# Kernel tuning notes

Measured on AMD Instinct MI355X. Metric: run time of the kernel, lower is better.

The kernel has to match this reference:

```python
import jax, jax.numpy as jnp
import numpy as np

B, S, D = 8, 1024, 768
H = 12
DH = D // H  # 64
SCALE = 1.0 / (D ** 0.5)  # module scales by full embedding_dim, not head_dim


def setup_inputs() -> dict:
    key = jax.random.key(0)
    ks = jax.random.split(key, 7)
    std = 1.0 / np.sqrt(D)
    return {
        "x": jax.random.normal(ks[0], (B, S, D), dtype=jnp.float32),
        "Wq": jax.random.uniform(ks[1], (D, D), jnp.float32, -std, std),
        "bq": jax.random.uniform(ks[2], (D,), jnp.float32, -std, std),
        "Wk": jax.random.uniform(ks[3], (D, D), jnp.float32, -std, std),
        "bk": jax.random.uniform(ks[4], (D,), jnp.float32, -std, std),
        "Wv": jax.random.uniform(ks[5], (D, D), jnp.float32, -std, std),
        "bv": jax.random.uniform(ks[6], (D,), jnp.float32, -std, std),
    }


def reference(x, Wq, bq, Wk, bk, Wv, bv):
    b, s, d = x.shape
    # projections; torch.chunk(dim=-1) == reshape last dim to [H, DH]
    q = (x @ Wq + bq).reshape(b, s, H, DH)
    k = (x @ Wk + bk).reshape(b, s, H, DH)
    v = (x @ Wv + bv).reshape(b, s, H, DH)
    # per-head scores [b, h, s, s], scaled by sqrt(embedding_dim) per source
    scores = jnp.einsum("bqhd,bkhd->bhqk", q, k) * SCALE
    attn = jax.nn.softmax(scores, axis=-1)
    out = jnp.einsum("bhqk,bkhd->bqhd", attn, v)
    # concat heads back along last dim (order matches chunk order)
    return out.reshape(b, s, d)
```

## Files before the change

kernel.cpp:

```cpp
#include <hip/hip_runtime.h>
#include <cstdint>
#include <cstddef>

typedef unsigned short u16;
typedef unsigned int u32;
typedef unsigned char u8;

using bfx8 = __attribute__((ext_vector_type(8))) __bf16;
using floatx16 = __attribute__((ext_vector_type(16))) float;

static constexpr int kS = 1024;
static constexpr int kD = 768;
static constexpr int kH = 12;
static constexpr int kDH = 64;
#define SCALE 0.036084391824351614f

__device__ __forceinline__ u16 f2bf(float f) {
    u32 u = __float_as_uint(f);
    return (u16)((u + 0x7fffu + ((u >> 16) & 1u)) >> 16);
}

__device__ __forceinline__ void gld16(const void* g, void* l) {
    __builtin_amdgcn_global_load_lds(
        (__attribute__((address_space(1))) const u32*)g,
        (__attribute__((address_space(3))) u32*)l, 16, 0, 0);
}

__global__ __launch_bounds__(256) void cvt_x(const float* __restrict__ x, u16* __restrict__ xb) {
    int i = (blockIdx.x * 256 + threadIdx.x) * 4;
    float4 v = *(const float4*)(x + i);
    u32 lo = (u32)f2bf(v.x) | ((u32)f2bf(v.y) << 16);
    u32 hi = (u32)f2bf(v.z) | ((u32)f2bf(v.w) << 16);
    *(uint2*)(xb + i) = make_uint2(lo, hi);
}

__global__ __launch_bounds__(256) void cvt_w(const float* __restrict__ w0, const float* __restrict__ w1,
                                             const float* __restrict__ w2, u16* __restrict__ wt) {
    __shared__ float t[32][33];
    const float* W = blockIdx.z == 0 ? w0 : (blockIdx.z == 1 ? w1 : w2);
    u16* dst = wt + (size_t)blockIdx.z * kD * kD;
    int k0 = blockIdx.x * 32, n0 = blockIdx.y * 32;
    int tx = threadIdx.x, ty = threadIdx.y;
#pragma unroll
    for (int j = 0; j < 4; j++)
        t[ty + j * 8][tx] = W[(size_t)(k0 + ty + j * 8) * kD + n0 + tx];
    __syncthreads();
#pragma unroll
    for (int j = 0; j < 4; j++)
        dst[(size_t)(n0 + ty + j * 8) * kD + k0 + tx] = f2bf(t[tx][ty + j * 8]);
}

__global__ __launch_bounds__(256) void proj(const u16* __restrict__ xb, const u16* __restrict__ wt,
                                            const float* __restrict__ bq, const float* __restrict__ bk,
                                            const float* __restrict__ bvp,
                                            u16* __restrict__ qb, u16* __restrict__ kb, u16* __restrict__ vt) {
    __shared__ u16 As[128 * 64];
    __shared__ u16 Bs[128 * 64];
    int m0 = blockIdx.x * 128;
    int n0g = blockIdx.y * 128;
    int t = threadIdx.x;
    int w = t >> 6, lane = t & 63;
    int l31 = lane & 31, hi = lane >> 5;
    int wm = (w & 1) * 64, wn = (w >> 1) * 64;
    int rloc8 = lane >> 3, p8 = lane & 7;
    int chw = p8 ^ rloc8;
    const u16* Brow = wt + (size_t)n0g * kD;
    int swz = l31 & 7;
    floatx16 acc[2][2] = {};
    for (int ks = 0; ks < kD; ks += 64) {
        __syncthreads();
#pragma unroll
        for (int i = 0; i < 4; i++) {
            int j = w * 4 + i;
            int r = 8 * j + rloc8;
            gld16(xb + (size_t)(m0 + r) * kD + ks + chw * 8, &As[j * 512]);
            gld16(Brow + (size_t)r * kD + ks + chw * 8, &Bs[j * 512]);
        }
        __syncthreads();
#pragma unroll
        for (int s = 0; s < 4; s++) {
            int tc = ((s * 2 + hi) ^ swz) * 8;
            bfx8 a[2], bf[2];
#pragma unroll
            for (int i = 0; i < 2; i++) {
                a[i] = *(const bfx8*)&As[(wm + i * 32 + l31) * 64 + tc];
                bf[i] = *(const bfx8*)&Bs[(wn + i * 32 + l31) * 64 + tc];
            }
#pragma unroll
            for (int i = 0; i < 2; i++)
#pragma unroll
                for (int j = 0; j < 2; j++)
                    acc[i][j] = __builtin_amdgcn_mfma_f32_32x32x16_bf16(a[i], bf[j], acc[i][j], 0, 0, 0);
        }
    }
    int zz = blockIdx.y / 6;
    int nl0 = (blockIdx.y - zz * 6) * 128;
    const float* bias = zz == 0 ? bq : (zz == 1 ? bk : bvp);
    float mul = zz == 0 ? SCALE : 1.0f;
#pragma unroll
    for (int j = 0; j < 2; j++) {
        int nl = nl0 + wn + j * 32 + l31;
        float bb = bias[nl];
#pragma unroll
        for (int i = 0; i < 2; i++) {
            int mbase = m0 + wm + i * 32 + 4 * hi;
            if (zz < 2) {
                u16* dst = zz == 0 ? qb : kb;
#pragma unroll
                for (int reg = 0; reg < 16; reg++) {
                    int m = mbase + (reg & 3) + 8 * (reg >> 2);
                    dst[(size_t)m * kD + nl] = f2bf((acc[i][j][reg] + bb) * mul);
                }
            } else {
                int hh = nl >> 6, dh = nl & 63;
#pragma unroll
                for (int g = 0; g < 4; g++) {
                    int m = mbase + 8 * g;
                    int bi = m >> 10, s = m & 1023;
                    u32 lo = (u32)f2bf(acc[i][j][4 * g + 0] + bb) | ((u32)f2bf(acc[i][j][4 * g + 1] + bb) << 16);
                    u32 h2 = (u32)f2bf(acc[i][j][4 * g + 2] + bb) | ((u32)f2bf(acc[i][j][4 * g + 3] + bb) << 16);
                    *(uint2*)&vt[(((size_t)bi * kH + hh) * kDH + dh) * kS + s] = make_uint2(lo, h2);
                }
            }
        }
    }
}

__global__ __launch_bounds__(256, 4) void attn(const u16* __restrict__ qb, const u16* __restrict__ kb,
                                               const u16* __restrict__ vt, float* __restrict__ out) {
    __shared__ u16 KPs[128 * 64];
    __shared__ u16 Vs[64 * 128];
    __shared__ float Lw[2][64];
    int q0 = blockIdx.x * 64;
    int bh = blockIdx.y;
    int b = bh / kH, h = bh % kH;
    int t = threadIdx.x, w = t >> 6, lane = t & 63;
    int l31 = lane & 31, hi = lane >> 5;
    int qh = w & 1, kh = w >> 1;

    bfx8 qf[4];
    {
        const u16* qrow = qb + (size_t)(b * kS + q0 + qh * 32 + l31) * kD + h * kDH + hi * 8;
#pragma unroll
        for (int f = 0; f < 4; f++) qf[f] = *(const bfx8*)(qrow + f * 16);
    }

    int qrl = qh * 32 + l31;
    int pswz = qrl & 15;
    float rsum = 0.f;
    floatx16 oacc = {};

    for (int kt = 0; kt < 8; kt++) {
        int kk0 = kt * 128;
        __syncthreads();
#pragma unroll
        for (int i = 0; i < 4; i++) {
            int jj = 4 * w + i;
            int r = 8 * jj + (lane >> 3);
            int c = (lane & 7) ^ ((lane >> 3) & 7);
            gld16(kb + (size_t)(b * kS + kk0 + r) * kD + h * kDH + c * 8, &KPs[jj * 512]);
        }
#pragma unroll
        for (int i = 0; i < 4; i++) {
            int jj = 4 * w + i;
            int r = 4 * jj + (lane >> 4);
            int c = (lane & 15) ^ (r & 15);
            gld16(vt + (((size_t)b * kH + h) * kDH + r) * kS + kk0 + c * 8, &Vs[jj * 512]);
        }
        __syncthreads();

        floatx16 sacc[2] = {};
#pragma unroll
        for (int s = 0; s < 4; s++) {
#pragma unroll
            for (int fm = 0; fm < 2; fm++) {
                int row = kh * 64 + fm * 32 + l31;
                int tc = ((s * 2 + hi) ^ (l31 & 7)) * 8;
                bfx8 ak = *(const bfx8*)&KPs[row * 64 + tc];
                sacc[fm] = __builtin_amdgcn_mfma_f32_32x32x16_bf16(ak, qf[s], sacc[fm], 0, 0, 0);
            }
        }
        __syncthreads();

        u8* prow = (u8*)KPs + qrl * 256;
#pragma unroll
        for (int fm = 0; fm < 2; fm++) {
#pragma unroll
            for (int g = 0; g < 4; g++) {
                float p0 = __expf(sacc[fm][4 * g + 0]);
                float p1 = __expf(sacc[fm][4 * g + 1]);
                float p2 = __expf(sacc[fm][4 * g + 2]);
                float p3 = __expf(sacc[fm][4 * g + 3]);
                rsum += (p0 + p1) + (p2 + p3);
                u32 lo = (u32)f2bf(p0) | ((u32)f2bf(p1) << 16);
                u32 h2 = (u32)f2bf(p2) | ((u32)f2bf(p3) << 16);
                int c16 = kh * 8 + fm * 4 + g;
                *(uint2*)(prow + ((c16 ^ pswz) * 2 + hi) * 8) = make_uint2(lo, h2);
            }
        }
        __syncthreads();

#pragma unroll
        for (int s = 0; s < 8; s++) {
            bfx8 ap = *(const bfx8*)(prow + ((s * 2 + hi) ^ pswz) * 16);
            bfx8 bv = *(const bfx8*)((const u8*)Vs + (kh * 32 + l31) * 256 + (((s * 2 + hi) ^ (l31 & 15)) * 16));
            oacc = __builtin_amdgcn_mfma_f32_32x32x16_bf16(ap, bv, oacc, 0, 0, 0);
        }
    }

    rsum += __shfl_xor(rsum, 32, 64);
    if (lane < 32) Lw[kh][qh * 32 + lane] = rsum;
    __syncthreads();
#pragma unroll
    for (int g = 0; g < 4; g++) {
#pragma unroll
        for (int r2 = 0; r2 < 4; r2++) {
            int qloc = qh * 32 + r2 + 8 * g + 4 * hi;
            float linv = 1.0f / (Lw[0][qloc] + Lw[1][qloc]);
            out[(size_t)(b * kS + q0 + qloc) * kD + h * kDH + kh * 32 + l31] = oacc[4 * g + r2] * linv;
        }
    }
}

extern "C" void kernel_launch(void* const* d_in, const int* in_sizes, int n_in,
                              void* d_out, int out_size, void* d_ws, size_t ws_size,
                              hipStream_t stream) {
    const float* x  = (const float*)d_in[0];
    const float* Wq = (const float*)d_in[1];
    const float* bq = (const float*)d_in[2];
    const float* Wk = (const float*)d_in[3];
    const float* bk = (const float*)d_in[4];
    const float* Wv = (const float*)d_in[5];
    const float* bv = (const float*)d_in[6];
    float* out = (float*)d_out;

    u16* ws = (u16*)d_ws;
    u16* xb = ws;
    u16* wt = xb + 6291456;
    u16* qb = wt + 1769472;
    u16* kb = qb + 6291456;
    u16* vt = kb + 6291456;

    cvt_x<<<dim3(6144), dim3(256), 0, stream>>>(x, xb);
    cvt_w<<<dim3(24, 24, 3), dim3(32, 8), 0, stream>>>(Wq, Wk, Wv, wt);
    proj<<<dim3(64, 18), dim3(256), 0, stream>>>(xb, wt, bq, bk, bv, qb, kb, vt);
    attn<<<dim3(16, 96), dim3(256), 0, stream>>>(qb, kb, vt, out);
}
```

Before: 186.6 us.

## Double-buffer projection GEMM and keep attention probabilities in registers

The projection kernel now uses two LDS buffers, so the global-to-LDS load of the next K slice overlaps the MFMA work on the current one, with one barrier per step instead of two. The attention kernel is restructured so each wave owns 32 queries across all 128 keys of a tile. The exponentiated scores are converted directly into the bf16 A-operand registers of the P·V MFMA, which removes the LDS round trip for P and two barriers per tile. To make that register layout line up, V is written in a permuted sequence order during projection. Blocks now cover 128 queries with a lower occupancy hint, trading more registers per thread for less LDS traffic and synchronisation.

```diff
diff --git a/kernel.cpp b/kernel.cpp
--- a/kernel.cpp
+++ b/kernel.cpp
@@ -54,8 +54,10 @@
                                             const float* __restrict__ bq, const float* __restrict__ bk,
                                             const float* __restrict__ bvp,
                                             u16* __restrict__ qb, u16* __restrict__ kb, u16* __restrict__ vt) {
-    __shared__ u16 As[128 * 64];
-    __shared__ u16 Bs[128 * 64];
+    __shared__ u16 As0[128 * 64];
+    __shared__ u16 Bs0[128 * 64];
+    __shared__ u16 As1[128 * 64];
+    __shared__ u16 Bs1[128 * 64];
     int m0 = blockIdx.x * 128;
     int n0g = blockIdx.y * 128;
     int t = threadIdx.x;
@@ -67,32 +69,49 @@
     const u16* Brow = wt + (size_t)n0g * kD;
     int swz = l31 & 7;
     floatx16 acc[2][2] = {};
-    for (int ks = 0; ks < kD; ks += 64) {
-        __syncthreads();
+
+    auto STAGE = [&](u16* Ad, u16* Bd, int ks) {
 #pragma unroll
         for (int i = 0; i < 4; i++) {
             int j = w * 4 + i;
             int r = 8 * j + rloc8;
-            gld16(xb + (size_t)(m0 + r) * kD + ks + chw * 8, &As[j * 512]);
-            gld16(Brow + (size_t)r * kD + ks + chw * 8, &Bs[j * 512]);
-        }
-        __syncthreads();
+            gld16(xb + (size_t)(m0 + r) * kD + ks + chw * 8, Ad + j * 512);
+            gld16(Brow + (size_t)r * kD + ks + chw * 8, Bd + j * 512);
+        }
+    };
+    auto COMP = [&](const u16* Ad, const u16* Bd) {
 #pragma unroll
         for (int s = 0; s < 4; s++) {
             int tc = ((s * 2 + hi) ^ swz) * 8;
             bfx8 a[2], bf[2];
 #pragma unroll
             for (int i = 0; i < 2; i++) {
-                a[i] = *(const bfx8*)&As[(wm + i * 32 + l31) * 64 + tc];
-                bf[i] = *(const bfx8*)&Bs[(wn + i * 32 + l31) * 64 + tc];
+                a[i] = *(const bfx8*)&Ad[(wm + i * 32 + l31) * 64 + tc];
+                bf[i] = *(const bfx8*)&Bd[(wn + i * 32 + l31) * 64 + tc];
             }
 #pragma unroll
             for (int i = 0; i < 2; i++)
 #pragma unroll
-                for (int j = 0; j < 2; j++)
-                    acc[i][j] = __builtin_amdgcn_mfma_f32_32x32x16_bf16(a[i], bf[j], acc[i][j], 0, 0, 0);
-        }
-    }
+                for (int j2 = 0; j2 < 2; j2++)
+                    acc[i][j2] = __builtin_amdgcn_mfma_f32_32x32x16_bf16(a[i], bf[j2], acc[i][j2], 0, 0, 0);
+        }
+    };
+
+    STAGE(As0, Bs0, 0);
+    __syncthreads();
+    for (int kk = 0; kk < 5; kk++) {
+        STAGE(As1, Bs1, 64 + 128 * kk);
+        COMP(As0, Bs0);
+        __syncthreads();
+        STAGE(As0, Bs0, 128 + 128 * kk);
+        COMP(As1, Bs1);
+        __syncthreads();
+    }
+    STAGE(As1, Bs1, 704);
+    COMP(As0, Bs0);
+    __syncthreads();
+    COMP(As1, Bs1);
+
     int zz = blockIdx.y / 6;
     int nl0 = (blockIdx.y - zz * 6) * 128;
     const float* bias = zz == 0 ? bq : (zz == 1 ? bk : bvp);
@@ -115,7 +134,7 @@
                 int hh = nl >> 6, dh = nl & 63;
 #pragma unroll
                 for (int g = 0; g < 4; g++) {
-                    int m = mbase + 8 * g;
+                    int m = (m0 + wm + i * 32) + 4 * (g & 1) + 8 * hi + 16 * (g >> 1);
                     int bi = m >> 10, s = m & 1023;
                     u32 lo = (u32)f2bf(acc[i][j][4 * g + 0] + bb) | ((u32)f2bf(acc[i][j][4 * g + 1] + bb) << 16);
                     u32 h2 = (u32)f2bf(acc[i][j][4 * g + 2] + bb) | ((u32)f2bf(acc[i][j][4 * g + 3] + bb) << 16);
@@ -126,29 +145,27 @@
     }
 }
 
-__global__ __launch_bounds__(256, 4) void attn(const u16* __restrict__ qb, const u16* __restrict__ kb,
+__global__ __launch_bounds__(256, 3) void attn(const u16* __restrict__ qb, const u16* __restrict__ kb,
                                                const u16* __restrict__ vt, float* __restrict__ out) {
-    __shared__ u16 KPs[128 * 64];
+    __shared__ u16 Ks[128 * 64];
     __shared__ u16 Vs[64 * 128];
-    __shared__ float Lw[2][64];
-    int q0 = blockIdx.x * 64;
+    __shared__ float Lw[128];
+    int q0 = blockIdx.x * 128;
     int bh = blockIdx.y;
     int b = bh / kH, h = bh % kH;
     int t = threadIdx.x, w = t >> 6, lane = t & 63;
     int l31 = lane & 31, hi = lane >> 5;
-    int qh = w & 1, kh = w >> 1;
+    int swz = l31 & 7;
 
     bfx8 qf[4];
     {
-        const u16* qrow = qb + (size_t)(b * kS + q0 + qh * 32 + l31) * kD + h * kDH + hi * 8;
+        const u16* qrow = qb + (size_t)(b * kS + q0 + w * 32 + l31) * kD + h * kDH + hi * 8;
 #pragma unroll
         for (int f = 0; f < 4; f++) qf[f] = *(const bfx8*)(qrow + f * 16);
     }
 
-    int qrl = qh * 32 + l31;
-    int pswz = qrl & 15;
     float rsum = 0.f;
-    floatx16 oacc = {};
+    floatx16 oacc[2] = {};
 
     for (int kt = 0; kt < 8; kt++) {
         int kk0 = kt * 128;
@@ -158,7 +175,7 @@
             int jj = 4 * w + i;
             int r = 8 * jj + (lane >> 3);
             int c = (lane & 7) ^ ((lane >> 3) & 7);
-            gld16(kb + (size_t)(b * kS + kk0 + r) * kD + h * kDH + c * 8, &KPs[jj * 512]);
+            gld16(kb + (size_t)(b * kS + kk0 + r) * kD + h * kDH + c * 8, &Ks[jj * 512]);
         }
 #pragma unroll
         for (int i = 0; i < 4; i++) {
@@ -169,55 +186,55 @@
         }
         __syncthreads();
 
-        floatx16 sacc[2] = {};
-#pragma unroll
-        for (int s = 0; s < 4; s++) {
-#pragma unroll
-            for (int fm = 0; fm < 2; fm++) {
-                int row = kh * 64 + fm * 32 + l31;
-                int tc = ((s * 2 + hi) ^ (l31 & 7)) * 8;
-                bfx8 ak = *(const bfx8*)&KPs[row * 64 + tc];
-                sacc[fm] = __builtin_amdgcn_mfma_f32_32x32x16_bf16(ak, qf[s], sacc[fm], 0, 0, 0);
-            }
-        }
-        __syncthreads();
-
-        u8* prow = (u8*)KPs + qrl * 256;
-#pragma unroll
-        for (int fm = 0; fm < 2; fm++) {
-#pragma unroll
-            for (int g = 0; g < 4; g++) {
-                float p0 = __expf(sacc[fm][4 * g + 0]);
-                float p1 = __expf(sacc[fm][4 * g + 1]);
-                float p2 = __expf(sacc[fm][4 * g + 2]);
-                float p3 = __expf(sacc[fm][4 * g + 3]);
-                rsum += (p0 + p1) + (p2 + p3);
-                u32 lo = (u32)f2bf(p0) | ((u32)f2bf(p1) << 16);
-                u32 h2 = (u32)f2bf(p2) | ((u32)f2bf(p3) << 16);
-                int c16 = kh * 8 + fm * 4 + g;
-                *(uint2*)(prow + ((c16 ^ pswz) * 2 + hi) * 8) = make_uint2(lo, h2);
-            }
-        }
-        __syncthreads();
+        floatx16 sacc[4] = {};
+#pragma unroll
+        for (int s2 = 0; s2 < 4; s2++) {
+#pragma unroll
+            for (int fm = 0; fm < 4; fm++) {
+                bfx8 ak = *(const bfx8*)&Ks[(fm * 32 + l31) * 64 + ((s2 * 2 + hi) ^ swz) * 8];
+                sacc[fm] = __builtin_amdgcn_mfma_f32_32x32x16_bf16(ak, qf[s2], sacc[fm], 0, 0, 0);
+            }
+        }
+
+        bfx8 pa[4][2];
+#pragma unroll
+        for (int fm = 0; fm < 4; fm++) {
+#pragma unroll
+            for (int hh = 0; hh < 2; hh++) {
+                bfx8 pv;
+#pragma unroll
+                for (int jj = 0; jj < 8; jj++) {
+                    float e = __expf(sacc[fm][8 * hh + jj]);
+                    rsum += e;
+                    pv[jj] = (__bf16)e;
+                }
+                pa[fm][hh] = pv;
+            }
+        }
 
 #pragma unroll
         for (int s = 0; s < 8; s++) {
-            bfx8 ap = *(const bfx8*)(prow + ((s * 2 + hi) ^ pswz) * 16);
-            bfx8 bv = *(const bfx8*)((const u8*)Vs + (kh * 32 + l31) * 256 + (((s * 2 + hi) ^ (l31 & 15)) * 16));
-            oacc = __builtin_amdgcn_mfma_f32_32x32x16_bf16(ap, bv, oacc, 0, 0, 0);
+#pragma unroll
+            for (int db = 0; db < 2; db++) {
+                bfx8 bv = *(const bfx8*)((const u8*)Vs + (db * 32 + l31) * 256 + (((s * 2 + hi) ^ (l31 & 15)) * 16));
+                oacc[db] = __builtin_amdgcn_mfma_f32_32x32x16_bf16(pa[s >> 1][s & 1], bv, oacc[db], 0, 0, 0);
+            }
         }
     }
 
     rsum += __shfl_xor(rsum, 32, 64);
-    if (lane < 32) Lw[kh][qh * 32 + lane] = rsum;
+    if (lane < 32) Lw[w * 32 + lane] = rsum;
     __syncthreads();
 #pragma unroll
     for (int g = 0; g < 4; g++) {
 #pragma unroll
         for (int r2 = 0; r2 < 4; r2++) {
-            int qloc = qh * 32 + r2 + 8 * g + 4 * hi;
-            float linv = 1.0f / (Lw[0][qloc] + Lw[1][qloc]);
-            out[(size_t)(b * kS + q0 + qloc) * kD + h * kDH + kh * 32 + l31] = oacc[4 * g + r2] * linv;
+            int qloc = w * 32 + 4 * hi + r2 + 8 * g;
+            float linv = 1.0f / Lw[qloc];
+#pragma unroll
+            for (int db = 0; db < 2; db++) {
+                out[(size_t)(b * kS + q0 + qloc) * kD + h * kDH + db * 32 + l31] = oacc[db][4 * g + r2] * linv;
+            }
         }
     }
 }
@@ -244,5 +261,5 @@
     cvt_x<<<dim3(6144), dim3(256), 0, stream>>>(x, xb);
     cvt_w<<<dim3(24, 24, 3), dim3(32, 8), 0, stream>>>(Wq, Wk, Wv, wt);
     proj<<<dim3(64, 18), dim3(256), 0, stream>>>(xb, wt, bq, bk, bv, qb, kb, vt);
-    attn<<<dim3(16, 96), dim3(256), 0, stream>>>(qb, kb, vt, out);
-}
+    attn<<<dim3(8, 96), dim3(256), 0, stream>>>(qb, kb, vt, out);
+}
```

Measured after the change: 169.9 us. 9.0% less time.
